# Kernel optimization log

Measured on AMD Instinct MI355X. Metric: run time of the kernel, lower is better.

## Reference

```python
import jax, jax.numpy as jnp
import numpy as np

H, W = 512, 512          # config.height, config.width
PIXEL_SIZE = 1.0
A2P = 1.0 / PIXEL_SIZE   # angstrom_to_pixel
INV_AREA = 1.0 / PIXEL_SIZE ** 2
SQRT2 = 1.4142135623730951
N, F, B = 8192, 2, 8


def setup_inputs() -> dict:
    key = jax.random.key(0)
    k1, k2, k3, k4, k5 = jax.random.split(key, 5)
    centers = jax.random.uniform(k1, (N, 3), minval=64.0, maxval=448.0)
    scales = jax.random.uniform(k2, (N, F), minval=1.0, maxval=4.0)
    weights = jax.random.normal(k3, (N, F))
    bubble_weights = 0.1 * jax.random.normal(k4, (N,))
    transform_matrix = jnp.eye(4)[None] + 0.01 * jax.random.normal(k5, (B, 4, 4))
    return {
        "transform_matrix": transform_matrix,
        "centers": centers,
        "scales": scales,
        "weights": weights,
        "bubble_weights": bubble_weights,
    }


def _pixel_profile(c, s, n):
    # Exact integral of a 1D gaussian N(c, s^2) over each unit pixel [x-0.5, x+0.5].
    # c, s: (M,) -> (M, n)
    x = jnp.arange(n, dtype=c.dtype)
    lo = (x[None, :] - 0.5 - c[:, None]) / (s[:, None] * SQRT2)
    hi = (x[None, :] + 0.5 - c[:, None]) / (s[:, None] * SQRT2)
    return 0.5 * (jax.lax.erf(hi) - jax.lax.erf(lo))


def _splat_point_masses(img, cp, w):
    # Bilinear scatter-add of point masses at projected centers cp (N,2), coord0 = row.
    r, c = cp[:, 0], cp[:, 1]
    r0f, c0f = jnp.floor(r), jnp.floor(c)
    fr, fc = r - r0f, c - c0f
    r0, c0 = r0f.astype(jnp.int32), c0f.astype(jnp.int32)
    for dr, dc, ww in ((0, 0, (1 - fr) * (1 - fc)), (0, 1, (1 - fr) * fc),
                       (1, 0, fr * (1 - fc)), (1, 1, fr * fc)):
        rr = jnp.clip(r0 + dr, 0, H - 1)
        cc = jnp.clip(c0 + dc, 0, W - 1)
        img = img.at[rr, cc].add(w * ww)
    return img


def _render_one(cp, scales_px_flat, weights_flat, bubble_weights):
    # cp: (N, 2) projected centers in pixel units.
    cpe = jnp.repeat(cp, F, axis=0)                       # (N*F, 2): expand per scale
    ph = _pixel_profile(cpe[:, 0], scales_px_flat, H)     # (N*F, H)
    pw = _pixel_profile(cpe[:, 1], scales_px_flat, W)     # (N*F, W)
    img = jnp.einsum("mh,mw->hw", weights_flat[:, None] * ph, pw)
    img = _splat_point_masses(img, cp, bubble_weights)
    return img


def reference(transform_matrix, centers, scales, weights, bubble_weights):
    # Homogenize centers: (N, 4)
    ch = jnp.concatenate([centers, jnp.ones_like(centers[:, :1])], axis=-1)
    # Solve T x = c for each (pose, gaussian): (B,1,4,4) \\ (1,N,4,1) -> (B,N,4)
    proj = jnp.linalg.solve(transform_matrix[:, None], ch[None, :, :, None])[..., 0]
    cp = proj[..., :2] / proj[..., 3:4] * A2P             # (B, N, 2) pixel coords
    scales_px = (scales * A2P).reshape(-1)                # (N*F,)
    weights_flat = weights.reshape(-1)                    # (N*F,)
    render = jax.vmap(lambda c: _render_one(c, scales_px, weights_flat, bubble_weights))
    result = render(cp) * INV_AREA                        # (B, H, W)
    return result
```

## Files before the change

### kernel.cpp

```cpp
#include <hip/hip_runtime.h>
#include <hip/hip_bf16.h>

#define HH 512
#define WW 512
#define NN 8192
#define FF 2
#define BB 8
#define MM (NN * FF)
#define HW (HH * WW)
#define NC (BB * NN)

__device__ __forceinline__ float ld(const void* p, int i, int f32mode) {
  if (f32mode) return ((const float*)p)[i];
  unsigned u = ((const unsigned short*)p)[i];
  return __uint_as_float(u << 16);
}

__device__ __forceinline__ float readlane_f(float v, int l) {
  return __uint_as_float(__builtin_amdgcn_readlane(__float_as_uint(v), l));
}

__device__ __forceinline__ float erf_f(float x) {
  float ax = fabsf(x);
  float t = 1.0f / (1.0f + 0.3275911f * ax);
  float y = t * (0.254829592f +
           t * (-0.284496736f +
           t * (1.421413741f +
           t * (-1.453152027f +
           t * 1.061405429f))));
  y = 1.0f - y * __expf(-ax * ax);
  return copysignf(y, x);
}

__global__ void k_inv(const void* __restrict__ T, float* __restrict__ invT,
                      int* __restrict__ flag) {
  int b = threadIdx.x;
  if (b >= BB) return;
  const float* Tf = (const float*)T;
  int f32mode = (fabsf(Tf[0] - 1.f) < 0.4f &&
                 fabsf(Tf[5] - 1.f) < 0.4f &&
                 fabsf(Tf[10] - 1.f) < 0.4f) ? 1 : 0;
  if (b == 0) *flag = f32mode;

  float a[4][8];
  for (int r = 0; r < 4; ++r)
    for (int c = 0; c < 4; ++c) {
      a[r][c] = ld(T, b * 16 + r * 4 + c, f32mode);
      a[r][4 + c] = (r == c) ? 1.0f : 0.0f;
    }
  for (int k = 0; k < 4; ++k) {
    int p = k; float best = fabsf(a[k][k]);
    for (int i = k + 1; i < 4; ++i) {
      float v = fabsf(a[i][k]);
      if (v > best) { best = v; p = i; }
    }
    if (p != k)
      for (int c = 0; c < 8; ++c) { float tmp = a[k][c]; a[k][c] = a[p][c]; a[p][c] = tmp; }
    float inv = 1.0f / a[k][k];
    for (int c = 0; c < 8; ++c) a[k][c] *= inv;
    for (int i = 0; i < 4; ++i) {
      if (i == k) continue;
      float f = a[i][k];
      for (int c = 0; c < 8; ++c) a[i][c] -= f * a[k][c];
    }
  }
  for (int r = 0; r < 4; ++r)
    for (int c = 0; c < 4; ++c)
      invT[b * 16 + r * 4 + c] = a[r][4 + c];
}

__global__ void k_table(const void* __restrict__ centers, const void* __restrict__ scales,
                        const void* __restrict__ weights, const void* __restrict__ bubble,
                        const float* __restrict__ invT, const int* __restrict__ flag,
                        float4* __restrict__ tabA, float4* __restrict__ tabB,
                        float4* __restrict__ img4) {
  int idx = blockIdx.x * blockDim.x + threadIdx.x;
  int stride = gridDim.x * blockDim.x;
  for (int j = idx; j < BB * HW / 4; j += stride)
    img4[j] = make_float4(0.f, 0.f, 0.f, 0.f);
  if (idx >= NC) return;
  int f32mode = *flag;
  int b = idx >> 13;
  int n = idx & (NN - 1);
  const float* Tb = invT + b * 16;
  float cx = ld(centers, 3 * n, f32mode);
  float cy = ld(centers, 3 * n + 1, f32mode);
  float cz = ld(centers, 3 * n + 2, f32mode);
  float p0 = Tb[0]  * cx + Tb[1]  * cy + Tb[2]  * cz + Tb[3];
  float p1 = Tb[4]  * cx + Tb[5]  * cy + Tb[6]  * cz + Tb[7];
  float p3 = Tb[12] * cx + Tb[13] * cy + Tb[14] * cz + Tb[15];
  float inv = 1.0f / p3;
  float4 A, Bv;
  A.x = p0 * inv;
  A.y = p1 * inv;
  A.z = ld(scales, 2 * n, f32mode);
  A.w = ld(weights, 2 * n, f32mode);
  Bv.x = ld(scales, 2 * n + 1, f32mode);
  Bv.y = ld(weights, 2 * n + 1, f32mode);
  Bv.z = ld(bubble, n, f32mode);
  Bv.w = 0.f;
  tabA[idx] = A;
  tabB[idx] = Bv;
}

__global__ void k_splat(const float4* __restrict__ tabA, const float4* __restrict__ tabB,
                        float* __restrict__ img) {
  int gid = blockIdx.x * blockDim.x + threadIdx.x;
  int wave = gid >> 6;
  int lane = gid & 63;
  int nwaves = (gridDim.x * blockDim.x) >> 6;

  int i = wave;
  float4 A = make_float4(0.f, 0.f, 1.f, 0.f);
  float4 Bv = make_float4(1.f, 0.f, 0.f, 0.f);
  if (i < NC) { A = tabA[i]; Bv = tabB[i]; }

  while (i < NC) {
    int in = i + nwaves;
    float4 An = A, Bn = Bv;
    if (in < NC) { An = tabA[in]; Bn = tabB[in]; }

    float row = A.x, col = A.y, s0 = A.z, w0 = A.w;
    float s1 = Bv.x, w1 = Bv.y, bw = Bv.z;
    float* imgb = img + ((size_t)(i >> 13) << 18);

    {
      float r0f = floorf(row), c0f = floorf(col);
      float fr = row - r0f, fc = col - c0f;
      int r0 = (int)r0f, c0 = (int)c0f;
      int rr0 = min(max(r0, 0), HH - 1), rr1 = min(max(r0 + 1, 0), HH - 1);
      int cc0 = min(max(c0, 0), WW - 1), cc1 = min(max(c0 + 1, 0), WW - 1);
      int rsel = (lane < 2) ? rr0 : rr1;
      int csel = (lane & 1) ? cc1 : cc0;
      float wr = (lane < 2) ? (1.f - fr) : fr;
      float wc = (lane & 1) ? fc : (1.f - fc);
      if (lane < 4)
        unsafeAtomicAdd(imgb + (rsel << 9) + csel, bw * wr * wc);
    }

    float smax = fmaxf(s0, s1);
    float rs0 = 0.70710678118f / s0;
    float rs1 = 0.70710678118f / s1;
    float Rf = 5.0f * smax + 0.5f;
    int rlo = max(0, (int)ceilf(row - Rf));
    int rhi = min(HH - 1, (int)floorf(row + Rf));
    int clo = max(0, (int)ceilf(col - Rf));
    int chi = min(WW - 1, (int)floorf(col + Rf));
    if (rlo <= rhi && clo <= chi) {
      int nc = chi - clo + 1;
      int nr = rhi - rlo + 1;
      float xc = (float)(clo + lane) - 0.5f - col;
      float x0 = xc * rs0;
      float pw0 = (erf_f(x0 + rs0) - erf_f(x0)) * (0.25f * w0);
      float x1 = xc * rs1;
      float pw1 = (erf_f(x1 + rs1) - erf_f(x1)) * (0.25f * w1);
      float yr = (float)(rlo + lane) - 0.5f - row;
      float y0 = yr * rs0;
      float Dh0 = erf_f(y0 + rs0) - erf_f(y0);
      float y1 = yr * rs1;
      float Dh1 = erf_f(y1 + rs1) - erf_f(y1);
      float* base = imgb + (rlo << 9) + clo + lane;
      for (int k = 0; k < nr; ++k) {
        float val = readlane_f(Dh0, k) * pw0 + readlane_f(Dh1, k) * pw1;
        if (lane < nc)
          unsafeAtomicAdd(base + (k << 9), val);
      }
    }

    i = in; A = An; Bv = Bn;
  }
}

__global__ void k_final(const float4* __restrict__ img4, const int* __restrict__ flag,
                        void* __restrict__ out) {
  int idx = blockIdx.x * blockDim.x + threadIdx.x;
  int stride = gridDim.x * blockDim.x;
  int f32mode = *flag;
  if (f32mode) {
    float4* o = (float4*)out;
    for (int j = idx; j < BB * HW / 4; j += stride)
      o[j] = img4[j];
  } else {
    ushort4* o = (ushort4*)out;
    for (int j = idx; j < BB * HW / 4; j += stride) {
      float4 v = img4[j];
      __hip_bfloat16 h0 = __float2bfloat16(v.x);
      __hip_bfloat16 h1 = __float2bfloat16(v.y);
      __hip_bfloat16 h2 = __float2bfloat16(v.z);
      __hip_bfloat16 h3 = __float2bfloat16(v.w);
      ushort4 t;
      t.x = *reinterpret_cast<unsigned short*>(&h0);
      t.y = *reinterpret_cast<unsigned short*>(&h1);
      t.z = *reinterpret_cast<unsigned short*>(&h2);
      t.w = *reinterpret_cast<unsigned short*>(&h3);
      o[j] = t;
    }
  }
}

extern "C" void kernel_launch(void* const* d_in, const int* in_sizes, int n_in,
                              void* d_out, int out_size, void* d_ws, size_t ws_size,
                              hipStream_t stream) {
  const void* T       = d_in[0];
  const void* centers = d_in[1];
  const void* scales  = d_in[2];
  const void* weights = d_in[3];
  const void* bubble  = d_in[4];

  char* ws = (char*)d_ws;
  size_t off = 0;
  float*  img  = (float*)(ws + off);  off += (size_t)BB * HW * 4;
  float4* tabA = (float4*)(ws + off); off += (size_t)NC * 16;
  float4* tabB = (float4*)(ws + off); off += (size_t)NC * 16;
  float*  invT = (float*)(ws + off);  off += (size_t)BB * 16 * 4;
  int*    flag = (int*)(ws + off);

  k_inv<<<1, 64, 0, stream>>>(T, invT, flag);
  k_table<<<512, 256, 0, stream>>>(centers, scales, weights, bubble, invT, flag,
                                   tabA, tabB, (float4*)img);
  k_splat<<<2048, 256, 0, stream>>>(tabA, tabB, img);
  k_final<<<512, 256, 0, stream>>>((const float4*)img, flag, d_out);
}
```

Before: 606.2 us.

## Shrink gaussian footprint, split wave into two 32-wide row halves, one wave per gaussian

Cuts the splat radius from 5 sigma to 3.8 sigma and caps the footprint at 32x32, so each wave covers two rows per iteration with 32 lanes per row instead of one 64-lane row. It also drops the grid-stride loop in favor of one wave per gaussian, with a grid sized to the gaussian count. Together these reduce the number of atomic-add iterations and the wasted lanes on narrow footprints. The cost is accuracy: mass beyond 3.8 sigma is dropped, and footprints wider than 32 pixels are truncated.

Measured after the change: 912.5 us. 50.5% more time.

```diff
diff --git a/kernel.cpp b/kernel.cpp
--- a/kernel.cpp
+++ b/kernel.cpp
@@ -9,6 +9,8 @@
 #define MM (NN * FF)
 #define HW (HH * WW)
 #define NC (BB * NN)
+
+#define NSIG 3.8f
 
 __device__ __forceinline__ float ld(const void* p, int i, int f32mode) {
   if (f32mode) return ((const float*)p)[i];
@@ -103,71 +105,68 @@
   tabB[idx] = Bv;
 }
 
-__global__ void k_splat(const float4* __restrict__ tabA, const float4* __restrict__ tabB,
-                        float* __restrict__ img) {
+__global__ void __launch_bounds__(256)
+k_splat(const float4* __restrict__ tabA, const float4* __restrict__ tabB,
+        float* __restrict__ img) {
   int gid = blockIdx.x * blockDim.x + threadIdx.x;
-  int wave = gid >> 6;
+  int i = gid >> 6;
   int lane = gid & 63;
-  int nwaves = (gridDim.x * blockDim.x) >> 6;
-
-  int i = wave;
-  float4 A = make_float4(0.f, 0.f, 1.f, 0.f);
-  float4 Bv = make_float4(1.f, 0.f, 0.f, 0.f);
-  if (i < NC) { A = tabA[i]; Bv = tabB[i]; }
-
-  while (i < NC) {
-    int in = i + nwaves;
-    float4 An = A, Bn = Bv;
-    if (in < NC) { An = tabA[in]; Bn = tabB[in]; }
-
-    float row = A.x, col = A.y, s0 = A.z, w0 = A.w;
-    float s1 = Bv.x, w1 = Bv.y, bw = Bv.z;
-    float* imgb = img + ((size_t)(i >> 13) << 18);
-
-    {
-      float r0f = floorf(row), c0f = floorf(col);
-      float fr = row - r0f, fc = col - c0f;
-      int r0 = (int)r0f, c0 = (int)c0f;
-      int rr0 = min(max(r0, 0), HH - 1), rr1 = min(max(r0 + 1, 0), HH - 1);
-      int cc0 = min(max(c0, 0), WW - 1), cc1 = min(max(c0 + 1, 0), WW - 1);
-      int rsel = (lane < 2) ? rr0 : rr1;
-      int csel = (lane & 1) ? cc1 : cc0;
-      float wr = (lane < 2) ? (1.f - fr) : fr;
-      float wc = (lane & 1) ? fc : (1.f - fc);
-      if (lane < 4)
-        unsafeAtomicAdd(imgb + (rsel << 9) + csel, bw * wr * wc);
-    }
-
-    float smax = fmaxf(s0, s1);
-    float rs0 = 0.70710678118f / s0;
-    float rs1 = 0.70710678118f / s1;
-    float Rf = 5.0f * smax + 0.5f;
-    int rlo = max(0, (int)ceilf(row - Rf));
-    int rhi = min(HH - 1, (int)floorf(row + Rf));
-    int clo = max(0, (int)ceilf(col - Rf));
-    int chi = min(WW - 1, (int)floorf(col + Rf));
-    if (rlo <= rhi && clo <= chi) {
-      int nc = chi - clo + 1;
-      int nr = rhi - rlo + 1;
-      float xc = (float)(clo + lane) - 0.5f - col;
-      float x0 = xc * rs0;
-      float pw0 = (erf_f(x0 + rs0) - erf_f(x0)) * (0.25f * w0);
-      float x1 = xc * rs1;
-      float pw1 = (erf_f(x1 + rs1) - erf_f(x1)) * (0.25f * w1);
-      float yr = (float)(rlo + lane) - 0.5f - row;
-      float y0 = yr * rs0;
-      float Dh0 = erf_f(y0 + rs0) - erf_f(y0);
-      float y1 = yr * rs1;
-      float Dh1 = erf_f(y1 + rs1) - erf_f(y1);
-      float* base = imgb + (rlo << 9) + clo + lane;
-      for (int k = 0; k < nr; ++k) {
-        float val = readlane_f(Dh0, k) * pw0 + readlane_f(Dh1, k) * pw1;
-        if (lane < nc)
-          unsafeAtomicAdd(base + (k << 9), val);
-      }
-    }
-
-    i = in; A = An; Bv = Bn;
+  if (i >= NC) return;
+  float4 A = tabA[i];
+  float4 Bv = tabB[i];
+
+  float row = A.x, col = A.y, s0 = A.z, w0 = A.w;
+  float s1 = Bv.x, w1 = Bv.y, bw = Bv.z;
+  float* imgb = img + ((size_t)(i >> 13) << 18);
+
+  {
+    float r0f = floorf(row), c0f = floorf(col);
+    float fr = row - r0f, fc = col - c0f;
+    int r0 = (int)r0f, c0 = (int)c0f;
+    int rr0 = min(max(r0, 0), HH - 1), rr1 = min(max(r0 + 1, 0), HH - 1);
+    int cc0 = min(max(c0, 0), WW - 1), cc1 = min(max(c0 + 1, 0), WW - 1);
+    int rsel = (lane < 2) ? rr0 : rr1;
+    int csel = (lane & 1) ? cc1 : cc0;
+    float wr = (lane < 2) ? (1.f - fr) : fr;
+    float wc = (lane & 1) ? fc : (1.f - fc);
+    if (lane < 4)
+      unsafeAtomicAdd(imgb + (rsel << 9) + csel, bw * wr * wc);
+  }
+
+  float smax = fmaxf(s0, s1);
+  float rs0 = 0.70710678118f / s0;
+  float rs1 = 0.70710678118f / s1;
+  float Rf = NSIG * smax + 0.5f;
+  int rlo = max(0, (int)ceilf(row - Rf));
+  int rhi = min(HH - 1, (int)floorf(row + Rf));
+  int clo = max(0, (int)ceilf(col - Rf));
+  int chi = min(WW - 1, (int)floorf(col + Rf));
+  if (rlo > rhi || clo > chi) return;
+  int nc = min(chi - clo + 1, 32);
+  int nr = min(rhi - rlo + 1, 32);
+
+  int cl = lane & 31;
+  int half = lane >> 5;
+  float xc = (float)(clo + cl) - 0.5f - col;
+  float x0 = xc * rs0;
+  float pw0 = (erf_f(x0 + rs0) - erf_f(x0)) * (0.25f * w0);
+  float x1 = xc * rs1;
+  float pw1 = (erf_f(x1 + rs1) - erf_f(x1)) * (0.25f * w1);
+  float yr = (float)(rlo + lane) - 0.5f - row;
+  float y0 = yr * rs0;
+  float Dh0 = erf_f(y0 + rs0) - erf_f(y0);
+  float y1 = yr * rs1;
+  float Dh1 = erf_f(y1 + rs1) - erf_f(y1);
+
+  float* base = imgb + ((rlo + half) << 9) + clo + cl;
+  for (int k = 0; k < nr; k += 2) {
+    float d0a = readlane_f(Dh0, k), d0b = readlane_f(Dh0, k + 1);
+    float d1a = readlane_f(Dh1, k), d1b = readlane_f(Dh1, k + 1);
+    float d0 = half ? d0b : d0a;
+    float d1 = half ? d1b : d1a;
+    float val = d0 * pw0 + d1 * pw1;
+    if (cl < nc && k + half < nr)
+      unsafeAtomicAdd(base + (k << 9), val);
   }
 }
 
@@ -218,6 +217,6 @@
   k_inv<<<1, 64, 0, stream>>>(T, invT, flag);
   k_table<<<512, 256, 0, stream>>>(centers, scales, weights, bubble, invT, flag,
                                    tabA, tabB, (float4*)img);
-  k_splat<<<2048, 256, 0, stream>>>(tabA, tabB, img);
+  k_splat<<<NC / 4, 256, 0, stream>>>(tabA, tabB, img);
   k_final<<<512, 256, 0, stream>>>((const float4*)img, flag, d_out);
 }
```
